# Performance work log

Hardware: AMD Instinct MI355X
Metric: run time of the kernel (lower is better)

Reference implementation:

```python
import jax, jax.numpy as jnp
import numpy as np


def conv2d(x, w, groups=1, pad=0):
    # x: [N,C,H,W], w: [O, C//groups, kh, kw]
    return jax.lax.conv_general_dilated(
        x, w, window_strides=(1, 1), padding=[(pad, pad), (pad, pad)],
        dimension_numbers=("NCHW", "OIHW", "NCHW"), feature_group_count=groups)


def l2norm(x, eps=1e-12):
    # torch F.normalize over last dim: x / max(||x||_2, eps)
    n = jnp.sqrt(jnp.sum(x * x, axis=-1, keepdims=True))
    return x / jnp.maximum(n, eps)


def setup_inputs() -> dict:
    key = jax.random.key(0)
    dim, heads, b, H, W = 48, 8, 2, 256, 256
    ks = jax.random.split(key, 20)
    rn = lambda k, shp, s: (jax.random.normal(k, shp, dtype=jnp.float32) * s)
    return {
        "x1": rn(ks[0], (b, dim, H, W), 1.0),
        "x2": rn(ks[1], (b, dim, H, W), 1.0),
        "t1": jnp.ones((heads, 1, 1), jnp.float32),
        "t2": jnp.ones((heads, 1, 1), jnp.float32),
        "qkv1_w": rn(ks[2], (dim * 3, dim, 1, 1), 0.05),
        "qkv1_dw": rn(ks[3], (dim * 3, 1, 3, 3), 0.05),
        "qkv2_w": rn(ks[4], (dim * 3, dim, 1, 1), 0.05),
        "qkv2_dw": rn(ks[5], (dim * 3, 1, 3, 3), 0.05),
        "mid1_w": rn(ks[6], (dim, dim, 1, 1), 0.05),
        "mid2_w": rn(ks[7], (dim, dim, 1, 1), 0.05),
        "pE_w": rn(ks[8], (dim * 8, dim * 2, 1, 1), 0.05),
        "pE_dw": rn(ks[9], (dim * 8, 1, 3, 3), 0.05),
        "pE1_w": rn(ks[10], (dim * 4, dim, 1, 1), 0.05),
        "pE1_dw": rn(ks[11], (dim * 4, 1, 3, 3), 0.05),
        "pE2_w": rn(ks[12], (dim * 4, dim, 1, 1), 0.05),
        "pE2_dw": rn(ks[13], (dim * 4, 1, 3, 3), 0.05),
        "po1_w": rn(ks[14], (dim * 2, dim * 4, 1, 1), 0.05),
        "po2_w": rn(ks[15], (dim * 2, dim * 4, 1, 1), 0.05),
    }


def reference(x1, x2, t1, t2, qkv1_w, qkv1_dw, qkv2_w, qkv2_dw,
              mid1_w, mid2_w, pE_w, pE_dw, pE1_w, pE1_dw,
              pE2_w, pE2_dw, po1_w, po2_w):
    b, c, h, w = x1.shape
    heads = t1.shape[0]
    ch = c // heads  # channels per head

    def to_heads(t):  # [b, c, h, w] -> [b, heads, ch, h*w]
        return t.reshape(b, heads, ch, h * w)

    qkv1 = conv2d(conv2d(x1, qkv1_w), qkv1_dw, groups=3 * c, pad=1)
    q1, k1, v1 = jnp.split(qkv1, 3, axis=1)
    qkv2 = conv2d(conv2d(x2, qkv2_w), qkv2_dw, groups=3 * c, pad=1)
    q2, k2, v2 = jnp.split(qkv2, 3, axis=1)

    q1, k1, v1 = to_heads(q1), to_heads(k1), to_heads(v1)
    q2, k2, v2 = to_heads(q2), to_heads(k2), to_heads(v2)
    q1, k1 = l2norm(q1), l2norm(k1)
    q2, k2 = l2norm(q2), l2norm(k2)

    # channel cross-attention: [b, heads, ch, ch]
    attn1 = jnp.einsum("bhcn,bhdn->bhcd", q2, k1) * t1
    attn2 = jnp.einsum("bhcn,bhdn->bhcd", q1, k2) * t2
    out1 = jnp.einsum("bhcd,bhdn->bhcn", jax.nn.softmax(attn1, axis=-1), v1)
    out2 = jnp.einsum("bhcd,bhdn->bhcn", jax.nn.softmax(attn2, axis=-1), v2)
    out1 = out1.reshape(b, c, h, w)
    out2 = out2.reshape(b, c, h, w)

    x1 = x1 + conv2d(out1, mid1_w)
    x2 = x2 + conv2d(out2, mid2_w)
    out = jnp.concatenate([x1, x2], axis=1)  # [b, 2c, h, w]

    g = conv2d(conv2d(out, pE_w), pE_dw, groups=8 * c, pad=1)  # [b, 8c, h, w]
    g1, g2 = jnp.split(g, 2, axis=1)
    x1 = jax.nn.gelu(g1, approximate=False) * conv2d(conv2d(x1, pE1_w), pE1_dw, groups=4 * c, pad=1)
    x2 = jax.nn.gelu(g2, approximate=False) * conv2d(conv2d(x2, pE2_w), pE2_dw, groups=4 * c, pad=1)

    return out + conv2d(x1, po1_w) + conv2d(x2, po2_w)
```

## Files before the change

### kernel.cpp

```cpp
#include <hip/hip_runtime.h>
#include <math.h>

#define HW_ 65536

typedef __attribute__((ext_vector_type(8))) short b16x8;
typedef __attribute__((ext_vector_type(4))) short b16x4;
typedef __attribute__((ext_vector_type(4))) float f32x4;

__device__ __forceinline__ unsigned short f2b(float f) {
    union { float f; unsigned u; } v; v.f = f;
    unsigned r = v.u + 0x7fffu + ((v.u >> 16) & 1u);
    return (unsigned short)(r >> 16);
}
__device__ __forceinline__ float b2f(unsigned short h) {
    union { unsigned u; float f; } v; v.u = ((unsigned)h) << 16; return v.f;
}
__device__ __forceinline__ float gelu_f(float x) {
    float t = 0.7978845608f * fmaf(0.044715f * x, x * x, x);
    float e = __expf(2.f * t);
    float th = 1.f - 2.f / (e + 1.f);
    return 0.5f * x * (1.f + th);
}

__device__ __forceinline__ float wave_reduce_sum(float v) {
    #pragma unroll
    for (int off = 32; off; off >>= 1) v += __shfl_down(v, off, 64);
    return v;
}

__device__ __forceinline__ size_t baddr(long px, int CC, int g) {
    return (((size_t)(px >> 4)) * CC + g) * 128 + ((size_t)(px & 15) << 3);
}

__global__ __launch_bounds__(256) void wprep_k(
    const float* __restrict__ q1w, const float* __restrict__ q2w,
    const float* __restrict__ m1w, const float* __restrict__ m2w,
    const float* __restrict__ pEw, const float* __restrict__ p1w,
    const float* __restrict__ p2w, const float* __restrict__ o1w,
    const float* __restrict__ o2w,
    const float* __restrict__ q1dw, const float* __restrict__ q2dw,
    const float* __restrict__ pEdw, const float* __restrict__ p1dw,
    const float* __restrict__ p2dw,
    unsigned short* __restrict__ wt, float* __restrict__ dwt)
{
    const int idx = blockIdx.x * 256 + threadIdx.x;
    if (idx < 135168) {
        const int base[8] = {0,9216,18432,21504,24576,61440,98304,116736};
        int s = 0;
        #pragma unroll
        for (int i = 1; i < 8; i++) if (idx >= base[i]) s = i;
        const int local = idx - base[s];
        float v = 0.f;
        if (s < 4) {
            const int m = local >> 6, k = local & 63;
            const float* src = (s == 0) ? q1w : (s == 1) ? q2w : (s == 2) ? m1w : m2w;
            if (k < 48) v = src[m * 48 + k];
        } else if (s < 6) {
            const int br = s - 4;
            const int m = local / 96, k = local % 96;
            if (m < 192) {
                v = pEw[(size_t)(br * 192 + m) * 96 + k];
            } else {
                const float* p12 = br ? p2w : p1w;
                const int lo = br * 48, m2 = m - 192;
                if (k >= lo && k < lo + 48) v = p12[m2 * 48 + (k - lo)];
            }
        } else {
            const int m = local / 192, k = local % 192;
            v = ((s == 6) ? o1w : o2w)[m * 192 + k];
        }
        wt[idx] = f2b(v);
    } else if (idx < 135168 + 9504) {
        const int d = idx - 135168;
        const int dbase[5] = {0,1296,2592,6048,7776};
        const int Cs[5] = {144,144,384,192,192};
        int s = 0;
        #pragma unroll
        for (int i = 1; i < 5; i++) if (d >= dbase[i]) s = i;
        const int local = d - dbase[s], C = Cs[s];
        const int t = local / C, c = local % C;
        const float* src = (s == 0) ? q1dw : (s == 1) ? q2dw : (s == 2) ? pEdw
                         : (s == 3) ? p1dw : p2dw;
        dwt[d] = src[c * 9 + t];
    }
}

template<int BM, int KC, int NT, int BSRC, int EPI, bool GRIDSWAP>
__global__ __launch_bounds__(256) void gemm_k(
    const unsigned short* __restrict__ B16,
    const float* __restrict__ Bf32, int Cin,
    const unsigned short* __restrict__ W16,
    unsigned short* __restrict__ out16, int CCo, int Coff,
    float* __restrict__ outf, const unsigned short* __restrict__ res)
{
    constexpr int MF = BM / 16;
    const int tid = threadIdx.x;
    const int lane = tid & 63, w = tid >> 6;
    const int lm = lane & 15, lk = lane >> 4;
    const int mb = GRIDSWAP ? blockIdx.x : blockIdx.y;
    const int pxblk = GRIDSWAP ? blockIdx.y : blockIdx.x;
    const int m0 = mb * BM;
    const long wavepx = ((long)pxblk * 4 + w) * (NT * 16);
    const long pxb0 = wavepx >> 4;

    f32x4 acc[NT][MF];
    #pragma unroll
    for (int nt = 0; nt < NT; nt++)
        #pragma unroll
        for (int m = 0; m < MF; m++)
            #pragma unroll
            for (int j = 0; j < 4; j++) acc[nt][m][j] = 0.f;

    #pragma unroll
    for (int kc = 0; kc < KC; kc++) {
        b16x8 a[MF];
        #pragma unroll
        for (int m = 0; m < MF; m++)
            a[m] = *(const b16x8*)&W16[(size_t)(m0 + m * 16 + lm) * (KC * 32) + kc * 32 + lk * 8];
        #pragma unroll
        for (int nt = 0; nt < NT; nt++) {
            b16x8 bb;
            if (BSRC == 0) {
                bb = *(const b16x8*)&B16[((pxb0 + nt) * (KC * 4) + (kc * 4 + lk)) * 128 + lm * 8];
            } else {
                const long px = wavepx + nt * 16 + lm;
                const int p = (int)(px & 65535), bat = (int)(px >> 16);
                #pragma unroll
                for (int j = 0; j < 8; j++) {
                    const int c = kc * 32 + lk * 8 + j;
                    float v = (c < Cin) ? Bf32[((size_t)(bat * Cin + c) << 16) + p] : 0.f;
                    bb[j] = (short)f2b(v);
                }
            }
            #pragma unroll
            for (int m = 0; m < MF; m++)
                acc[nt][m] = __builtin_amdgcn_mfma_f32_16x16x32_bf16(a[m], bb, acc[nt][m], 0, 0, 0);
        }
    }

    #pragma unroll
    for (int nt = 0; nt < NT; nt++) {
        const long px = wavepx + nt * 16 + lm;
        #pragma unroll
        for (int m = 0; m < MF; m++) {
            const int mrow = m * 16 + lk * 4;
            if (EPI == 0) {
                b16x4 o;
                #pragma unroll
                for (int j = 0; j < 4; j++) o[j] = (short)f2b(acc[nt][m][j]);
                const int ch = Coff + m0 + mrow;
                *(b16x4*)&out16[((pxb0 + nt) * CCo + (ch >> 3)) * 128 + lm * 8 + (ch & 7)] = o;
            } else if (EPI == 1) {
                const int p = (int)(px & 65535), bat = (int)(px >> 16);
                b16x4 r4 = *(const b16x4*)&res[((pxb0 + nt) * 12 + (mrow >> 3)) * 128 + lm * 8 + (mrow & 7)];
                #pragma unroll
                for (int j = 0; j < 4; j++)
                    outf[((size_t)(bat * 96 + mrow + j) << 16) + p]
                        = acc[nt][m][j] + b2f((unsigned short)r4[j]);
            } else {
                const int p = (int)(px & 65535), bat = (int)(px >> 16);
                #pragma unroll
                for (int j = 0; j < 4; j++) {
                    const size_t adr = ((size_t)(bat * 96 + mrow + j) << 16) + p;
                    outf[adr] += acc[nt][m][j];
                }
            }
        }
    }
}

__device__ __forceinline__ void unpack8(const uint4 u, float f[8]) {
    union { unsigned u; float f; } a;
    a.u = u.x << 16;         f[0] = a.f;
    a.u = u.x & 0xFFFF0000u; f[1] = a.f;
    a.u = u.y << 16;         f[2] = a.f;
    a.u = u.y & 0xFFFF0000u; f[3] = a.f;
    a.u = u.z << 16;         f[4] = a.f;
    a.u = u.z & 0xFFFF0000u; f[5] = a.f;
    a.u = u.w << 16;         f[6] = a.f;
    a.u = u.w & 0xFFFF0000u; f[7] = a.f;
}

__device__ __forceinline__ void dw_row4(
    float acc[4][8], const unsigned short* __restrict__ T,
    size_t cb, long lOff, long rOff, bool lval, bool rval,
    const float* __restrict__ wrow, int wstr)
{
    float w[3][8];
    #pragma unroll
    for (int tx = 0; tx < 3; tx++) {
        const float4 a = *(const float4*)(wrow + (size_t)tx * wstr);
        const float4 b = *(const float4*)(wrow + (size_t)tx * wstr + 4);
        w[tx][0] = a.x; w[tx][1] = a.y; w[tx][2] = a.z; w[tx][3] = a.w;
        w[tx][4] = b.x; w[tx][5] = b.y; w[tx][6] = b.z; w[tx][7] = b.w;
    }
    uint4 u[6];
    if (lval) u[0] = *(const uint4*)&T[cb + lOff];
    else      u[0] = make_uint4(0u, 0u, 0u, 0u);
    #pragma unroll
    for (int c = 0; c < 4; c++) u[c + 1] = *(const uint4*)&T[cb + (size_t)c * 8];
    if (rval) u[5] = *(const uint4*)&T[cb + rOff];
    else      u[5] = make_uint4(0u, 0u, 0u, 0u);

    #pragma unroll
    for (int d = 0; d < 6; d++) {
        float f[8];
        unpack8(u[d], f);
        #pragma unroll
        for (int tx = 0; tx < 3; tx++) {
            const int p = d - tx;
            if (p >= 0 && p < 4)
                #pragma unroll
                for (int j = 0; j < 8; j++)
                    acc[p][j] = fmaf(w[tx][j], f[j], acc[p][j]);
        }
    }
}

__global__ __launch_bounds__(256) void dw144_k(
    const unsigned short* __restrict__ in1, unsigned short* __restrict__ out1,
    const unsigned short* __restrict__ in2, unsigned short* __restrict__ out2,
    const float* __restrict__ dwt)
{
    const int z = blockIdx.z;
    const unsigned short* in = z ? in2 : in1;
    unsigned short* out = z ? out2 : out1;
    const float* wt = dwt + z * 1296;
    const int bx = blockIdx.x;
    const int sb = (bx & 7) * 288 + (bx >> 3);
    const int idx = sb * 256 + threadIdx.x;
    const int pbi = idx / 72;
    const int rem = idx - pbi * 72;
    const int g = rem >> 2, i = rem & 3;
    const long px0 = (long)pbi * 16 + i * 4;
    const int x0 = (int)(px0 & 255);
    const int y = (int)((px0 >> 8) & 255);
    const bool lval = x0 > 0, rval = x0 < 252;
    const int off = (int)(px0 & 15) * 8;
    const size_t cb0 = ((size_t)(px0 >> 4) * 18 + g) * 128 + off;
    const long lOff = (off == 0) ? (120 - 18 * 128) : -8;
    const long rOff = (off == 96) ? (18 * 128 - 96) : 32;
    const long dyStep = 16 * 18 * 128;

    float acc[4][8];
    #pragma unroll
    for (int p = 0; p < 4; p++)
        #pragma unroll
        for (int j = 0; j < 8; j++) acc[p][j] = 0.f;

    #pragma unroll
    for (int dy = -1; dy <= 1; dy++) {
        const int yy = y + dy;
        if ((unsigned)yy >= 256u) continue;
        const size_t cb = cb0 + (size_t)((long)dy * dyStep);
        dw_row4(acc, in, cb, lOff, rOff, lval, rval,
                wt + g * 8 + (size_t)(dy + 1) * 3 * 144, 144);
    }

    #pragma unroll
    for (int p = 0; p < 4; p++) {
        b16x8 o;
        #pragma unroll
        for (int j = 0; j < 8; j++) o[j] = (short)f2b(acc[p][j]);
        *(b16x8*)&out[cb0 + (size_t)p * 8] = o;
    }
}

__device__ __forceinline__ void dw_acc8(
    float acc[4][8], const unsigned short* __restrict__ T, int CC, int g,
    long px0, int y, int x0, const float* __restrict__ wt, int wstr)
{
    #pragma unroll
    for (int dy = -1; dy <= 1; dy++) {
        const int yy = y + dy;
        if ((unsigned)yy >= 256u) continue;
        float w[3][8];
        #pragma unroll
        for (int t = 0; t < 3; t++) {
            const float* wp = wt + (size_t)((dy + 1) * 3 + t) * wstr;
            const float4 a = *(const float4*)wp;
            const float4 b = *(const float4*)(wp + 4);
            w[t][0] = a.x; w[t][1] = a.y; w[t][2] = a.z; w[t][3] = a.w;
            w[t][4] = b.x; w[t][5] = b.y; w[t][6] = b.z; w[t][7] = b.w;
        }
        #pragma unroll
        for (int c = 0; c < 6; c++) {
            const int xx = x0 - 1 + c;
            b16x8 v;
            if ((unsigned)xx < 256u) {
                v = *(const b16x8*)&T[baddr(px0 + dy * 256 + (c - 1), CC, g)];
            } else {
                #pragma unroll
                for (int k = 0; k < 8; k++) v[k] = 0;
            }
            float f[8];
            #pragma unroll
            for (int k = 0; k < 8; k++) f[k] = b2f((unsigned short)v[k]);
            const int ilo = (c - 2 < 0) ? 0 : c - 2;
            const int ihi = (c < 3) ? c : 3;
            #pragma unroll
            for (int i = ilo; i <= ihi; i++)
                #pragma unroll
                for (int j = 0; j < 8; j++)
                    acc[i][j] = fmaf(w[c - i][j], f[j], acc[i][j]);
        }
    }
}

__global__ __launch_bounds__(256) void dwtail_k(
    const unsigned short* __restrict__ GH, unsigned short* __restrict__ Xg,
    const float* __restrict__ dwtG, const float* __restrict__ dwtH)
{
    const int bx = blockIdx.x;
    const int sb = (bx & 7) * 384 + (bx >> 3);
    const int idx = sb * 256 + threadIdx.x;
    const int pb = idx / 96;
    const int rem = idx - pb * 96;
    const int g = rem >> 2, i = rem & 3;
    const long px0 = (long)pb * 16 + i * 4;
    const int y = (int)((px0 & 65535) >> 8), x0 = (int)(px0 & 255);

    float aG[4][8], aH[4][8];
    #pragma unroll
    for (int a = 0; a < 4; a++)
        #pragma unroll
        for (int j = 0; j < 8; j++) { aG[a][j] = 0.f; aH[a][j] = 0.f; }
    dw_acc8(aG, GH, 48, g,      px0, y, x0, dwtG + g * 8, 384);
    dw_acc8(aH, GH, 48, 24 + g, px0, y, x0, dwtH + g * 8, 192);

    #pragma unroll
    for (int a = 0; a < 4; a++) {
        b16x8 o;
        #pragma unroll
        for (int j = 0; j < 8; j++)
            o[j] = (short)f2b(gelu_f(aG[a][j]) * aH[a][j]);
        *(b16x8*)&Xg[baddr(px0 + a, 24, g)] = o;
    }
}

__global__ __launch_bounds__(256) void attnA_k(
    const unsigned short* __restrict__ Q1, const unsigned short* __restrict__ Q2,
    float* __restrict__ part)
{
    const int tid = threadIdx.x;
    const int chunk = blockIdx.x, bh = blockIdx.y, a = blockIdx.z;
    const int b = bh >> 3, h = bh & 7;
    const unsigned* Qq = (const unsigned*)(a ? Q1 : Q2);
    const unsigned* Qk = (const unsigned*)(a ? Q2 : Q1);
    const int u0 = h * 3;
    const int cq = u0 >> 2, o = u0 & 3;
    const int ck = (24 + u0) >> 2;

    float dot[36], nq[6], nk[6];
    #pragma unroll
    for (int i = 0; i < 36; i++) dot[i] = 0.f;
    #pragma unroll
    for (int i = 0; i < 6; i++) { nq[i] = 0.f; nk[i] = 0.f; }

    #pragma unroll 1
    for (int r = 0; r < 8; r++) {
        const long px = (long)b * 65536 + chunk * 2048 + r * 256 + tid;
        const size_t rowu = ((size_t)(px >> 4)) * 18 * 64 + ((px & 15) << 2);
        const uint4 qa = *(const uint4*)&Qq[rowu + (size_t)cq * 64];
        const uint4 qb = *(const uint4*)&Qq[rowu + (size_t)(cq + 1) * 64];
        const uint4 ka = *(const uint4*)&Qk[rowu + (size_t)ck * 64];
        const uint4 kb = *(const uint4*)&Qk[rowu + (size_t)(ck + 1) * 64];
        unsigned uq[3], uk[3];
        if (o == 0)      { uq[0]=qa.x; uq[1]=qa.y; uq[2]=qa.z; uk[0]=ka.x; uk[1]=ka.y; uk[2]=ka.z; }
        else if (o == 1) { uq[0]=qa.y; uq[1]=qa.z; uq[2]=qa.w; uk[0]=ka.y; uk[1]=ka.z; uk[2]=ka.w; }
        else if (o == 2) { uq[0]=qa.z; uq[1]=qa.w; uq[2]=qb.x; uk[0]=ka.z; uk[1]=ka.w; uk[2]=kb.x; }
        else             { uq[0]=qa.w; uq[1]=qb.x; uq[2]=qb.y; uk[0]=ka.w; uk[1]=kb.x; uk[2]=kb.y; }
        float q[6], k[6];
        #pragma unroll
        for (int i = 0; i < 3; i++) {
            union { unsigned u; float f; } lo, hi;
            lo.u = uq[i] << 16; hi.u = uq[i] & 0xFFFF0000u;
            q[2 * i] = lo.f; q[2 * i + 1] = hi.f;
            lo.u = uk[i] << 16; hi.u = uk[i] & 0xFFFF0000u;
            k[2 * i] = lo.f; k[2 * i + 1] = hi.f;
        }
        #pragma unroll
        for (int c = 0; c < 6; c++) nq[c] = fmaf(q[c], q[c], nq[c]);
        #pragma unroll
        for (int d = 0; d < 6; d++) nk[d] = fmaf(k[d], k[d], nk[d]);
        #pragma unroll
        for (int c = 0; c < 6; c++)
            #pragma unroll
            for (int d = 0; d < 6; d++) dot[c * 6 + d] = fmaf(q[c], k[d], dot[c * 6 + d]);
    }

    __shared__ float red[4][48];
    const int lane = tid & 63, wid = tid >> 6;
    #pragma unroll
    for (int i = 0; i < 48; i++) {
        float v = (i < 36) ? dot[i] : (i < 42 ? nq[i - 36] : nk[i - 42]);
        v = wave_reduce_sum(v);
        if (!lane) red[wid][i] = v;
    }
    __syncthreads();
    if (tid < 48)
        part[((size_t)((a * 16 + bh) * 32 + chunk)) * 48 + tid]
            = red[0][tid] + red[1][tid] + red[2][tid] + red[3][tid];
}

__global__ void attnB_k(const float* __restrict__ part,
                        const float* __restrict__ t1, const float* __restrict__ t2,
                        float* __restrict__ att)
{
    const int abh = blockIdx.x, tid = threadIdx.x;
    const int a = abh >> 4, b = (abh >> 3) & 1, h = abh & 7;
    __shared__ float s[48];
    if (tid < 48) {
        float v = 0.f;
        for (int ch = 0; ch < 32; ch++) v += part[((size_t)abh * 32 + ch) * 48 + tid];
        s[tid] = v;
    }
    __syncthreads();
    if (tid < 6) {
        const int c = tid;
        const float tv = a ? t2[h] : t1[h];
        const float qn = fmaxf(sqrtf(s[36 + c]), 1e-12f);
        float raw[6];
        #pragma unroll
        for (int d = 0; d < 6; d++)
            raw[d] = tv * s[c * 6 + d] / (qn * fmaxf(sqrtf(s[42 + d]), 1e-12f));
        float m = raw[0];
        #pragma unroll
        for (int d = 1; d < 6; d++) m = fmaxf(m, raw[d]);
        float e[6], sum = 0.f;
        #pragma unroll
        for (int d = 0; d < 6; d++) { e[d] = expf(raw[d] - m); sum += e[d]; }
        const float inv = 1.f / sum;
        #pragma unroll
        for (int d = 0; d < 6; d++)
            att[((size_t)(a * 2 + b) * 8 + h) * 36 + c * 6 + d] = e[d] * inv;
    }
}

__global__ __launch_bounds__(256) void mid_k(
    const unsigned short* __restrict__ Q1, const unsigned short* __restrict__ Q2,
    const float* __restrict__ att,
    const float* __restrict__ x1, const float* __restrict__ x2,
    const unsigned short* __restrict__ Wm, unsigned short* __restrict__ D16p)
{
    const int br = blockIdx.y;
    const unsigned short* Qv = br ? Q2 : Q1;
    const float* x = br ? x2 : x1;
    const unsigned short* W16 = Wm + br * 3072;
    const float* attb = att + br * 576;
    const int boff = br * 48;

    __shared__ float atts[288];
    __shared__ unsigned short S[256][72];
    const int tid = threadIdx.x;
    const long px = (long)blockIdx.x * 256 + tid;
    const int bat = (int)(px >> 16);

    for (int i = tid; i < 288; i += 256) atts[i] = attb[bat * 288 + i];

    float v[48];
    #pragma unroll
    for (int i = 0; i < 6; i++) {
        b16x8 t = *(const b16x8*)&Qv[baddr(px, 18, 12 + i)];
        #pragma unroll
        for (int j = 0; j < 8; j++) v[i * 8 + j] = b2f((unsigned short)t[j]);
    }
    __syncthreads();

    #pragma unroll
    for (int h = 0; h < 8; h++) {
        unsigned short sh[6];
        #pragma unroll
        for (int c = 0; c < 6; c++) {
            float s = 0.f;
            #pragma unroll
            for (int d = 0; d < 6; d++) s = fmaf(atts[h * 36 + c * 6 + d], v[h * 6 + d], s);
            sh[c] = f2b(s);
        }
        #pragma unroll
        for (int i = 0; i < 3; i++) {
            unsigned packed = (unsigned)sh[2 * i] | ((unsigned)sh[2 * i + 1] << 16);
            *(unsigned*)&S[tid][h * 6 + 2 * i] = packed;
        }
    }
    #pragma unroll
    for (int i = 0; i < 8; i++) *(unsigned*)&S[tid][48 + 2 * i] = 0u;
    __syncthreads();

    const int lane = tid & 63, w = tid >> 6;
    const int lm = lane & 15, lk = lane >> 4;
    f32x4 acc[4][3];
    #pragma unroll
    for (int nt = 0; nt < 4; nt++)
        #pragma unroll
        for (int m = 0; m < 3; m++)
            #pragma unroll
            for (int j = 0; j < 4; j++) acc[nt][m][j] = 0.f;

    #pragma unroll
    for (int kc = 0; kc < 2; kc++) {
        b16x8 a[3];
        #pragma unroll
        for (int m = 0; m < 3; m++)
            a[m] = *(const b16x8*)&W16[(size_t)(m * 16 + lm) * 64 + kc * 32 + lk * 8];
        #pragma unroll
        for (int nt = 0; nt < 4; nt++) {
            b16x8 bb = *(const b16x8*)&S[w * 64 + nt * 16 + lm][kc * 32 + lk * 8];
            #pragma unroll
            for (int m = 0; m < 3; m++)
                acc[nt][m] = __builtin_amdgcn_mfma_f32_16x16x32_bf16(a[m], bb, acc[nt][m], 0, 0, 0);
        }
    }

    #pragma unroll
    for (int nt = 0; nt < 4; nt++) {
        const long px2 = (long)blockIdx.x * 256 + w * 64 + nt * 16 + lm;
        const int p2 = (int)(px2 & 65535);
        const long pxb2 = px2 >> 4;
        #pragma unroll
        for (int m = 0; m < 3; m++) {
            const int row = m * 16 + lk * 4;
            b16x4 o;
            #pragma unroll
            for (int j = 0; j < 4; j++) {
                float xv = x[((size_t)(bat * 48 + row + j) << 16) + p2];
                o[j] = (short)f2b(acc[nt][m][j] + xv);
            }
            const int ch = boff + row;
            *(b16x4*)&D16p[(pxb2 * 12 + (ch >> 3)) * 128 + lm * 8 + (ch & 7)] = o;
        }
    }
}

extern "C" void kernel_launch(void* const* d_in, const int* in_sizes, int n_in,
                              void* d_out, int out_size, void* d_ws, size_t ws_size,
                              hipStream_t stream) {
    const float* x1      = (const float*)d_in[0];
    const float* x2      = (const float*)d_in[1];
    const float* t1      = (const float*)d_in[2];
    const float* t2      = (const float*)d_in[3];
    const float* qkv1_w  = (const float*)d_in[4];
    const float* qkv1_dw = (const float*)d_in[5];
    const float* qkv2_w  = (const float*)d_in[6];
    const float* qkv2_dw = (const float*)d_in[7];
    const float* mid1_w  = (const float*)d_in[8];
    const float* mid2_w  = (const float*)d_in[9];
    const float* pE_w    = (const float*)d_in[10];
    const float* pE_dw   = (const float*)d_in[11];
    const float* pE1_w   = (const float*)d_in[12];
    const float* pE1_dw  = (const float*)d_in[13];
    const float* pE2_w   = (const float*)d_in[14];
    const float* pE2_dw  = (const float*)d_in[15];
    const float* po1_w   = (const float*)d_in[16];
    const float* po2_w   = (const float*)d_in[17];
    float* dout = (float*)d_out;
    char* ws = (char*)d_ws;

    unsigned short* D16p  = (unsigned short*)(ws + 0);
    unsigned short* QKVc1 = (unsigned short*)(ws + 25165824);
    unsigned short* QKVc2 = (unsigned short*)(ws + 62914560);
    unsigned short* Q1    = (unsigned short*)(ws + 100663296);
    unsigned short* Q2    = (unsigned short*)(ws + 138412032);
    unsigned short* GH    = (unsigned short*)(ws + 25165824);
    unsigned short* Xg    = (unsigned short*)(ws + 125829120);
    float*          PART  = (float*)(ws + 176160768);
    float*          ATT   = (float*)(ws + 176357376);
    unsigned short* W16   = (unsigned short*)(ws + 176361984);
    float*          DWT   = (float*)(ws + 176632320);

    const dim3 blk(256);

    wprep_k<<<dim3(566), blk, 0, stream>>>(
        qkv1_w, qkv2_w, mid1_w, mid2_w, pE_w, pE1_w, pE2_w, po1_w, po2_w,
        qkv1_dw, qkv2_dw, pE_dw, pE1_dw, pE2_dw, W16, DWT);

    gemm_k<144,2,2,1,0,false><<<dim3(1024,1), blk, 0, stream>>>(
        nullptr, x1, 48, W16, QKVc1, 18, 0, nullptr, nullptr);
    gemm_k<144,2,2,1,0,false><<<dim3(1024,1), blk, 0, stream>>>(
        nullptr, x2, 48, W16 + 9216, QKVc2, 18, 0, nullptr, nullptr);
    dw144_k<<<dim3(2304,1,2), blk, 0, stream>>>(QKVc1, Q1, QKVc2, Q2, DWT);

    attnA_k<<<dim3(32,16,2), blk, 0, stream>>>(Q1, Q2, PART);
    attnB_k<<<dim3(32), dim3(64), 0, stream>>>(PART, t1, t2, ATT);

    mid_k<<<dim3(512,2), blk, 0, stream>>>(Q1, Q2, ATT, x1, x2, W16 + 18432, D16p);

    for (int br = 0; br < 2; br++) {
        gemm_k<96,3,2,0,0,true><<<dim3(4,1024), blk, 0, stream>>>(
            D16p, nullptr, 0, W16 + 24576 + br * 36864, GH, 48, 0,
            nullptr, nullptr);
        dwtail_k<<<dim3(3072), blk, 0, stream>>>(
            GH, Xg, DWT + 2592 + br * 192, DWT + (br ? 7776 : 6048));
        if (br == 0)
            gemm_k<96,6,2,0,1,false><<<dim3(1024,1), blk, 0, stream>>>(
                Xg, nullptr, 0, W16 + 98304, nullptr, 0, 0, dout, D16p);
        else
            gemm_k<96,6,2,0,2,false><<<dim3(1024,1), blk, 0, stream>>>(
                Xg, nullptr, 0, W16 + 116736, nullptr, 0, 0, dout, nullptr);
    }
}
```

Baseline: 406.5 us.

## Pre-convert inputs to packed bf16 and reuse them in QKV GEMM and residual

Adds a kernel that converts x1 and x2 once into the packed bf16 pixel-block layout. The QKV GEMM then loads B fragments as vectors instead of doing strided fp32 scalar loads with per-element conversion. The mid kernel also reads the residual from this bf16 copy instead of from fp32. The two QKV branches now run back to back with their depthwise convs through one shared intermediate buffer, which shrinks the working set. The cost is an extra launch, an extra buffer write, and slightly lower residual precision because x is rounded to bf16 before the add.

```diff
diff --git a/kernel.cpp b/kernel.cpp
--- a/kernel.cpp
+++ b/kernel.cpp
@@ -85,7 +85,39 @@
     }
 }
 
-template<int BM, int KC, int NT, int BSRC, int EPI, bool GRIDSWAP>
+__global__ __launch_bounds__(256) void xcvt_k(
+    const float* __restrict__ x1, const float* __restrict__ x2,
+    unsigned short* __restrict__ Xb1, unsigned short* __restrict__ Xb2)
+{
+    const float* x = blockIdx.z ? x2 : x1;
+    unsigned short* Xb = blockIdx.z ? Xb2 : Xb1;
+    const int g = blockIdx.y;
+    const long pxb = (long)blockIdx.x * 256 + threadIdx.x;
+    const long px0 = pxb * 16;
+    const int bat = (int)(px0 >> 16);
+    const int p0 = (int)(px0 & 65535);
+    unsigned short* dst = Xb + (size_t)(pxb * 6 + g) * 128;
+    const float* sp0 = x + ((size_t)(bat * 48 + g * 8) << 16) + p0;
+
+    #pragma unroll
+    for (int q = 0; q < 4; q++) {
+        float vv[8][4];
+        #pragma unroll
+        for (int j = 0; j < 8; j++) {
+            float4 v = *(const float4*)(sp0 + ((size_t)j << 16) + q * 4);
+            vv[j][0] = v.x; vv[j][1] = v.y; vv[j][2] = v.z; vv[j][3] = v.w;
+        }
+        #pragma unroll
+        for (int p = 0; p < 4; p++) {
+            b16x8 o;
+            #pragma unroll
+            for (int j = 0; j < 8; j++) o[j] = (short)f2b(vv[j][p]);
+            *(b16x8*)&dst[(q * 4 + p) * 8] = o;
+        }
+    }
+}
+
+template<int BM, int KC, int NT, int BSRC, int EPI, bool GRIDSWAP, int CCB = KC * 4>
 __global__ __launch_bounds__(256) void gemm_k(
     const unsigned short* __restrict__ B16,
     const float* __restrict__ Bf32, int Cin,
@@ -121,7 +153,13 @@
         for (int nt = 0; nt < NT; nt++) {
             b16x8 bb;
             if (BSRC == 0) {
-                bb = *(const b16x8*)&B16[((pxb0 + nt) * (KC * 4) + (kc * 4 + lk)) * 128 + lm * 8];
+                const int kch = kc * 4 + lk;
+                if (CCB >= KC * 4 || kch < CCB) {
+                    bb = *(const b16x8*)&B16[((pxb0 + nt) * CCB + kch) * 128 + lm * 8];
+                } else {
+                    #pragma unroll
+                    for (int j = 0; j < 8; j++) bb[j] = 0;
+                }
             } else {
                 const long px = wavepx + nt * 16 + lm;
                 const int p = (int)(px & 65535), bat = (int)(px >> 16);
@@ -218,14 +256,9 @@
 }
 
 __global__ __launch_bounds__(256) void dw144_k(
-    const unsigned short* __restrict__ in1, unsigned short* __restrict__ out1,
-    const unsigned short* __restrict__ in2, unsigned short* __restrict__ out2,
-    const float* __restrict__ dwt)
-{
-    const int z = blockIdx.z;
-    const unsigned short* in = z ? in2 : in1;
-    unsigned short* out = z ? out2 : out1;
-    const float* wt = dwt + z * 1296;
+    const unsigned short* __restrict__ in, unsigned short* __restrict__ out,
+    const float* __restrict__ wt)
+{
     const int bx = blockIdx.x;
     const int sb = (bx & 7) * 288 + (bx >> 3);
     const int idx = sb * 256 + threadIdx.x;
@@ -440,12 +473,12 @@
 __global__ __launch_bounds__(256) void mid_k(
     const unsigned short* __restrict__ Q1, const unsigned short* __restrict__ Q2,
     const float* __restrict__ att,
-    const float* __restrict__ x1, const float* __restrict__ x2,
+    const unsigned short* __restrict__ Xb1, const unsigned short* __restrict__ Xb2,
     const unsigned short* __restrict__ Wm, unsigned short* __restrict__ D16p)
 {
     const int br = blockIdx.y;
     const unsigned short* Qv = br ? Q2 : Q1;
-    const float* x = br ? x2 : x1;
+    const unsigned short* Xb = br ? Xb2 : Xb1;
     const unsigned short* W16 = Wm + br * 3072;
     const float* attb = att + br * 576;
     const int boff = br * 48;
@@ -515,17 +548,15 @@
     #pragma unroll
     for (int nt = 0; nt < 4; nt++) {
         const long px2 = (long)blockIdx.x * 256 + w * 64 + nt * 16 + lm;
-        const int p2 = (int)(px2 & 65535);
         const long pxb2 = px2 >> 4;
         #pragma unroll
         for (int m = 0; m < 3; m++) {
             const int row = m * 16 + lk * 4;
+            b16x4 r4 = *(const b16x4*)&Xb[(pxb2 * 6 + (row >> 3)) * 128 + lm * 8 + (row & 7)];
             b16x4 o;
             #pragma unroll
-            for (int j = 0; j < 4; j++) {
-                float xv = x[((size_t)(bat * 48 + row + j) << 16) + p2];
-                o[j] = (short)f2b(acc[nt][m][j] + xv);
-            }
+            for (int j = 0; j < 4; j++)
+                o[j] = (short)f2b(acc[nt][m][j] + b2f((unsigned short)r4[j]));
             const int ch = boff + row;
             *(b16x4*)&D16p[(pxb2 * 12 + (ch >> 3)) * 128 + lm * 8 + (ch & 7)] = o;
         }
@@ -557,16 +588,17 @@
     char* ws = (char*)d_ws;
 
     unsigned short* D16p  = (unsigned short*)(ws + 0);
-    unsigned short* QKVc1 = (unsigned short*)(ws + 25165824);
-    unsigned short* QKVc2 = (unsigned short*)(ws + 62914560);
-    unsigned short* Q1    = (unsigned short*)(ws + 100663296);
-    unsigned short* Q2    = (unsigned short*)(ws + 138412032);
+    unsigned short* Xb1   = (unsigned short*)(ws + 25165824);
+    unsigned short* Xb2   = (unsigned short*)(ws + 38797312);
+    unsigned short* QKVc  = (unsigned short*)(ws + 51380224);
+    unsigned short* Q1    = (unsigned short*)(ws + 89128960);
+    unsigned short* Q2    = (unsigned short*)(ws + 126877696);
     unsigned short* GH    = (unsigned short*)(ws + 25165824);
     unsigned short* Xg    = (unsigned short*)(ws + 125829120);
-    float*          PART  = (float*)(ws + 176160768);
-    float*          ATT   = (float*)(ws + 176357376);
-    unsigned short* W16   = (unsigned short*)(ws + 176361984);
-    float*          DWT   = (float*)(ws + 176632320);
+    unsigned short* W16   = (unsigned short*)(ws + 176160768);
+    float*          DWT   = (float*)(ws + 176431104);
+    float*          PART  = (float*)(ws + 176469120);
+    float*          ATT   = (float*)(ws + 176665728);
 
     const dim3 blk(256);
 
@@ -574,28 +606,31 @@
         qkv1_w, qkv2_w, mid1_w, mid2_w, pE_w, pE1_w, pE2_w, po1_w, po2_w,
         qkv1_dw, qkv2_dw, pE_dw, pE1_dw, pE2_dw, W16, DWT);
 
-    gemm_k<144,2,2,1,0,false><<<dim3(1024,1), blk, 0, stream>>>(
-        nullptr, x1, 48, W16, QKVc1, 18, 0, nullptr, nullptr);
-    gemm_k<144,2,2,1,0,false><<<dim3(1024,1), blk, 0, stream>>>(
-        nullptr, x2, 48, W16 + 9216, QKVc2, 18, 0, nullptr, nullptr);
-    dw144_k<<<dim3(2304,1,2), blk, 0, stream>>>(QKVc1, Q1, QKVc2, Q2, DWT);
+    xcvt_k<<<dim3(32, 6, 2), blk, 0, stream>>>(x1, x2, Xb1, Xb2);
+
+    gemm_k<144,2,2,0,0,false,6><<<dim3(1024,1), blk, 0, stream>>>(
+        Xb1, nullptr, 0, W16, QKVc, 18, 0, nullptr, nullptr);
+    dw144_k<<<dim3(2304), blk, 0, stream>>>(QKVc, Q1, DWT);
+    gemm_k<144,2,2,0,0,false,6><<<dim3(1024,1), blk, 0, stream>>>(
+        Xb2, nullptr, 0, W16 + 9216, QKVc, 18, 0, nullptr, nullptr);
+    dw144_k<<<dim3(2304), blk, 0, stream>>>(QKVc, Q2, DWT + 1296);
 
     attnA_k<<<dim3(32,16,2), blk, 0, stream>>>(Q1, Q2, PART);
     attnB_k<<<dim3(32), dim3(64), 0, stream>>>(PART, t1, t2, ATT);
 
-    mid_k<<<dim3(512,2), blk, 0, stream>>>(Q1, Q2, ATT, x1, x2, W16 + 18432, D16p);
+    mid_k<<<dim3(512,2), blk, 0, stream>>>(Q1, Q2, ATT, Xb1, Xb2, W16 + 18432, D16p);
 
     for (int br = 0; br < 2; br++) {
-        gemm_k<96,3,2,0,0,true><<<dim3(4,1024), blk, 0, stream>>>(
+        gemm_k<96,3,2,0,0,true,12><<<dim3(4,1024), blk, 0, stream>>>(
             D16p, nullptr, 0, W16 + 24576 + br * 36864, GH, 48, 0,
             nullptr, nullptr);
         dwtail_k<<<dim3(3072), blk, 0, stream>>>(
             GH, Xg, DWT + 2592 + br * 192, DWT + (br ? 7776 : 6048));
         if (br == 0)
-            gemm_k<96,6,2,0,1,false><<<dim3(1024,1), blk, 0, stream>>>(
+            gemm_k<96,6,2,0,1,false,24><<<dim3(1024,1), blk, 0, stream>>>(
                 Xg, nullptr, 0, W16 + 98304, nullptr, 0, 0, dout, D16p);
         else
-            gemm_k<96,6,2,0,2,false><<<dim3(1024,1), blk, 0, stream>>>(
+            gemm_k<96,6,2,0,2,false,24><<<dim3(1024,1), blk, 0, stream>>>(
                 Xg, nullptr, 0, W16 + 116736, nullptr, 0, 0, dout, nullptr);
     }
 }
```

Result: slower. 428.0 us (+5.3%).
